# Performance work log

Hardware: AMD Instinct MI355X
Metric: run time of the kernel (lower is better)

The kernel has to match this reference:

```python
import jax, jax.numpy as jnp
from jax import lax
import numpy as np

KAPPA_S = 6.0
KAPPA_D = 5.0
POLICY_STRETCH = 2.0
VALUE_STRETCH = 1.0 / 32.0
VALUE_GAUGE = 0.2

RAW_PATTERNS = [
    [[0, 0, 0, 0, -5, 1, 1, 1, 1], [0, 0, 0, 0, -5, -5, -5, -5, -5], 0],
    [[0, 0, 0, 1, -5, 1, 1, 1, 0], [0, 0, 0, -5, -5, -5, -5, -5, 0], 0],
    [[0, 0, 1, 1, -5, 1, 1, 0, 0], [0, 0, -5, -5, -5, -5, -5, 0, 0], 0],
    [[0, 1, 1, 1, -5, 1, 0, 0, 0], [0, -5, -5, -5, -5, -5, 0, 0, 0], 0],
    [[1, 1, 1, 1, -5, 0, 0, 0, 0], [-5, -5, -5, -5, -5, 0, 0, 0, 0], 0],
    [[0, -5, 1, 1, 1, 1, 1, -5, 0], [0, 0, -5, -5, -5, -5, -5, 0, 0], -4],
]


def _all_3xnxn(p3):
    # Lay a 9-long 1D pattern (one per input channel) along the 4 line
    # directions (horizontal, vertical, two diagonals) of a 9x9 kernel.
    f = np.zeros((9, 9, 3, 4), np.float32)
    for ch in range(3):
        v = np.asarray(p3[ch], np.float32)
        f[4, :, ch, 0] = v                       # horizontal
        f[:, 4, ch, 1] = v                       # vertical
        for i in range(9):
            f[i, i, ch, 2] = v[i]                # main diagonal
            f[i, 8 - i, ch, 3] = v[i]            # anti diagonal
    return f


def _assemble_filters():
    # select_patterns: channel 0 -> [offense, defense, defense]; channel 1 -> [defense, offense, defense]
    patterns = []
    for off, de, bias in RAW_PATTERNS:
        patterns.append(([off, de, de], bias))
        patterns.append(([de, off, de], bias))
    filt = np.stack([_all_3xnxn(p) for p, _ in patterns], axis=3)  # (9,9,3,12,4)
    filt = np.reshape(filt, (9, 9, 3, -1))                          # filter idx = 4*pattern + direction
    biases = np.asarray([b for _, b in patterns for _ in range(4)], np.float32)
    return jnp.asarray(filt), jnp.asarray(biases)


def _safe_pow(x, p):
    # x >= 0 everywhere it is used; guards the grad of x**p (p<1) at x==0.
    pos = x > 0
    return jnp.where(pos, jnp.where(pos, x, 1.0) ** p, 0.0)


def setup_inputs() -> dict:
    key = jax.random.key(0)
    state = jax.random.normal(key, (4096, 19, 19, 3), dtype=jnp.float32)
    W, b = _assemble_filters()
    return {"state": state, "W": W, "b": b}


def reference(state, W, b):
    # detector: Conv2D 9x9, 48 filters, SAME padding, relu
    counts = jax.nn.relu(
        lax.conv_general_dilated(
            state, W, window_strides=(1, 1), padding="SAME",
            dimension_numbers=("NHWC", "HWIO", "NHWC"),
        ) + b
    )  # [B, N, N, 48]
    # peel: 3x3 conv with identity-center kernel, VALID padding == crop of 1
    core = counts[:, 1:-1, 1:-1, :]  # [B, N-2, N-2, 48]
    B, H, Wd, _ = core.shape
    # filter index = 8*shift + 4*channel + direction for the 40 line filters
    core40 = core[..., :40].reshape(B, H, Wd, 5, 2, 4)  # (shift, channel, direction)
    s = jnp.sum(core40 ** KAPPA_S, axis=3)               # sum over shifts -> [B,H,W,2,4]
    sd = jnp.sum(_safe_pow(s, KAPPA_D / KAPPA_S), axis=4)  # sum over directions -> [B,H,W,2]
    f = _safe_pow(sd, 1.0 / KAPPA_D)                     # [B,H,W,2]; [...,c] = field(channel c)
    f_cur, f_oth = f[..., 0], f[..., 1]
    logits = (f_cur + f_oth).reshape(B, -1)
    probs = jax.nn.softmax(POLICY_STRETCH * logits, axis=-1)
    raw_value = VALUE_GAUGE * (jnp.sum(f_cur, axis=(1, 2)) - jnp.sum(f_oth, axis=(1, 2)))
    value = jnp.tanh(VALUE_STRETCH * raw_value)
    return probs, value
```

## Files before the change

kernel.cpp:

```cpp
#include <hip/hip_runtime.h>
#include <math.h>


__device__ __forceinline__ float fpow(float x, float e) {
    float r = __builtin_amdgcn_exp2f(e * __builtin_amdgcn_logf(x));
    return (x > 0.f) ? r : 0.f;
}
__device__ __forceinline__ float fexp(float x) {
    return __builtin_amdgcn_exp2f(x * 1.44269504088896f);
}

#define SLAB 1024
#define C_OFF 729

__global__ __launch_bounds__(256) void topo_policy_value(
    const float* __restrict__ state,
    float* __restrict__ probs,
    float* __restrict__ value,
    int nb)
{
    __shared__ float2 l2[4 * SLAB];

    const int tid  = threadIdx.x;
    const int wv   = tid >> 6;
    const int lane = tid & 63;
    const int b    = blockIdx.x * 4 + wv;
    if (b >= nb) return;
    float2* s2 = l2 + wv * SLAB;

    const float* src = state + (size_t)b * (19 * 19 * 3);

    #pragma unroll
    for (int it = 0; it < 12; ++it) {
        int j = lane + it * 64;
        if (j < 729) {
            int py = j / 27, px = j - py * 27;
            int r = py - 4, c = px - 4;
            float l0 = 0.f, l1 = 0.f, lv = 0.f;
            if ((unsigned)r < 19u && (unsigned)c < 19u) {
                int o = 3 * (r * 19 + c);
                l0 = src[o]; l1 = src[o + 1]; lv = src[o + 2];
            }
            s2[j] = make_float2(fmaf(-5.f, l1 + lv, l0),
                                fmaf(-5.f, l0 + lv, l1));
        }
    }
    #pragma unroll
    for (int it = 0; it < 5; ++it) {
        int j = lane + it * 64;
        if (j < 289) {
            int y = j / 17, x = j - y * 17;
            int o = 3 * ((y + 1) * 19 + (x + 1));
            s2[C_OFF + j] = make_float2(6.f * src[o], 6.f * src[o + 1]);
        }
    }
    __builtin_amdgcn_s_waitcnt(0);
    __builtin_amdgcn_wave_barrier();

    float g[5], es[5];
    float dif = 0.f;
    #pragma unroll
    for (int k = 0; k < 5; ++k) {
        int p = lane + 64 * k;
        float gk = -3.0e38f;
        if (p < 289) {
            int y = p / 17, x = p - y * 17;
            float2 h = s2[C_OFF + p];
            int c0 = (y + 5) * 27 + (x + 1);
            int c1 = (y + 1) * 27 + (x + 5);
            int c2 = (y + 1) * 27 + (x + 1);
            int c3 = (y + 1) * 27 + (x + 9);
            float sd0 = 0.f, sd1 = 0.f;
            #define ORIENT(BASE, STEP)                                      \
            {                                                               \
                float2 e[9];                                                \
                _Pragma("unroll")                                           \
                for (int i = 0; i < 9; ++i) e[i] = s2[(BASE) + i * (STEP)]; \
                float wx = e[4].x + e[5].x + e[6].x + e[7].x + e[8].x;      \
                float wy = e[4].y + e[5].y + e[6].y + e[7].y + e[8].y;      \
                float t0 = 0.f, t1 = 0.f;                                   \
                _Pragma("unroll")                                           \
                for (int pp = 0; pp < 5; ++pp) {                            \
                    float a0 = fmaxf(wx - h.x, 0.f);                        \
                    float a1 = fmaxf(wy - h.y, 0.f);                        \
                    float q0 = a0 * a0, q1 = a1 * a1;                       \
                    t0 = fmaf(q0 * q0, q0, t0);                             \
                    t1 = fmaf(q1 * q1, q1, t1);                             \
                    if (pp < 4) {                                           \
                        wx += e[3 - pp].x - e[8 - pp].x;                    \
                        wy += e[3 - pp].y - e[8 - pp].y;                    \
                    }                                                       \
                }                                                           \
                sd0 += fpow(t0, 5.0f / 6.0f);                               \
                sd1 += fpow(t1, 5.0f / 6.0f);                               \
            }
            ORIENT(c0, 1)
            ORIENT(c1, 27)
            ORIENT(c2, 28)
            ORIENT(c3, 26)
            #undef ORIENT
            float fc = fpow(sd0, 0.2f);
            float fo = fpow(sd1, 0.2f);
            gk = 2.f * (fc + fo);
            dif += fc - fo;
        }
        g[k] = gk;
    }

    float M = fmaxf(fmaxf(fmaxf(g[0], g[1]), fmaxf(g[2], g[3])), g[4]);
    #pragma unroll
    for (int off = 32; off > 0; off >>= 1)
        M = fmaxf(M, __shfl_xor(M, off, 64));

    float S = 0.f;
    #pragma unroll
    for (int k = 0; k < 5; ++k) {
        es[k] = (g[k] > -1.0e38f) ? fexp(g[k] - M) : 0.f;
        S += es[k];
    }
    #pragma unroll
    for (int off = 32; off > 0; off >>= 1) S += __shfl_xor(S, off, 64);
    #pragma unroll
    for (int off = 32; off > 0; off >>= 1) dif += __shfl_xor(dif, off, 64);

    const float invS = __builtin_amdgcn_rcpf(S);
    float* pout = probs + (size_t)b * 289;
    #pragma unroll
    for (int k = 0; k < 5; ++k) {
        int p = lane + 64 * k;
        if (p < 289) pout[p] = es[k] * invS;
    }
    if (lane == 0) {
        float z = dif * (0.2f / 32.0f);
        float t = __builtin_amdgcn_exp2f(z * (2.0f * 1.44269504088896f));
        value[b] = (t - 1.f) * __builtin_amdgcn_rcpf(t + 1.f);
    }
}

extern "C" void kernel_launch(void* const* d_in, const int* in_sizes, int n_in,
                              void* d_out, int out_size, void* d_ws, size_t ws_size,
                              hipStream_t stream) {
    const float* state = (const float*)d_in[0];
    const int nb = in_sizes[0] / (19 * 19 * 3);
    float* probs = (float*)d_out;
    float* value = probs + (size_t)nb * 289;
    const int grid = (nb + 3) / 4;
    topo_policy_value<<<dim3(grid), dim3(256), 0, stream>>>(state, probs, value, nb);
}
```

Baseline: 84.29 us.

## Map one board per block with one thread per board position

```diff
diff --git a/kernel.cpp b/kernel.cpp
--- a/kernel.cpp
+++ b/kernel.cpp
@@ -13,26 +13,65 @@
 #define SLAB 1024
 #define C_OFF 729
 
-__global__ __launch_bounds__(256) void topo_policy_value(
+__device__ __forceinline__ float2 eval_pos(const float2* __restrict__ s2, int p)
+{
+    int y = p / 17, x = p - y * 17;
+    float2 h = s2[C_OFF + p];
+    int c0 = (y + 5) * 27 + (x + 1);
+    int c1 = (y + 1) * 27 + (x + 5);
+    int c2 = (y + 1) * 27 + (x + 1);
+    int c3 = (y + 1) * 27 + (x + 9);
+    float sd0 = 0.f, sd1 = 0.f;
+    #define ORIENT(BASE, STEP)                                      \
+    {                                                               \
+        float2 e[9];                                                \
+        _Pragma("unroll")                                           \
+        for (int i = 0; i < 9; ++i) e[i] = s2[(BASE) + i * (STEP)]; \
+        float wx = e[4].x + e[5].x + e[6].x + e[7].x + e[8].x;      \
+        float wy = e[4].y + e[5].y + e[6].y + e[7].y + e[8].y;      \
+        float t0 = 0.f, t1 = 0.f;                                   \
+        _Pragma("unroll")                                           \
+        for (int pp = 0; pp < 5; ++pp) {                            \
+            float a0 = fmaxf(wx - h.x, 0.f);                        \
+            float a1 = fmaxf(wy - h.y, 0.f);                        \
+            float q0 = a0 * a0, q1 = a1 * a1;                       \
+            t0 = fmaf(q0 * q0, q0, t0);                             \
+            t1 = fmaf(q1 * q1, q1, t1);                             \
+            if (pp < 4) {                                           \
+                wx += e[3 - pp].x - e[8 - pp].x;                    \
+                wy += e[3 - pp].y - e[8 - pp].y;                    \
+            }                                                       \
+        }                                                           \
+        sd0 += fpow(t0, 5.0f / 6.0f);                               \
+        sd1 += fpow(t1, 5.0f / 6.0f);                               \
+    }
+    ORIENT(c0, 1)
+    ORIENT(c1, 27)
+    ORIENT(c2, 28)
+    ORIENT(c3, 26)
+    #undef ORIENT
+    return make_float2(fpow(sd0, 0.2f), fpow(sd1, 0.2f));
+}
+
+__global__ __launch_bounds__(256, 6) void topo_policy_value(
     const float* __restrict__ state,
     float* __restrict__ probs,
     float* __restrict__ value,
     int nb)
 {
-    __shared__ float2 l2[4 * SLAB];
+    __shared__ float2 s2[SLAB];
+    __shared__ float red[4][3];
 
     const int tid  = threadIdx.x;
     const int wv   = tid >> 6;
     const int lane = tid & 63;
-    const int b    = blockIdx.x * 4 + wv;
-    if (b >= nb) return;
-    float2* s2 = l2 + wv * SLAB;
+    const int b    = blockIdx.x;
 
     const float* src = state + (size_t)b * (19 * 19 * 3);
 
     #pragma unroll
-    for (int it = 0; it < 12; ++it) {
-        int j = lane + it * 64;
+    for (int it = 0; it < 3; ++it) {
+        int j = tid + it * 256;
         if (j < 729) {
             int py = j / 27, px = j - py * 27;
             int r = py - 4, c = px - 4;
@@ -46,92 +85,57 @@
         }
     }
     #pragma unroll
-    for (int it = 0; it < 5; ++it) {
-        int j = lane + it * 64;
+    for (int it = 0; it < 2; ++it) {
+        int j = tid + it * 256;
         if (j < 289) {
             int y = j / 17, x = j - y * 17;
             int o = 3 * ((y + 1) * 19 + (x + 1));
             s2[C_OFF + j] = make_float2(6.f * src[o], 6.f * src[o + 1]);
         }
     }
-    __builtin_amdgcn_s_waitcnt(0);
-    __builtin_amdgcn_wave_barrier();
+    __syncthreads();
 
-    float g[5], es[5];
     float dif = 0.f;
-    #pragma unroll
-    for (int k = 0; k < 5; ++k) {
-        int p = lane + 64 * k;
-        float gk = -3.0e38f;
-        if (p < 289) {
-            int y = p / 17, x = p - y * 17;
-            float2 h = s2[C_OFF + p];
-            int c0 = (y + 5) * 27 + (x + 1);
-            int c1 = (y + 1) * 27 + (x + 5);
-            int c2 = (y + 1) * 27 + (x + 1);
-            int c3 = (y + 1) * 27 + (x + 9);
-            float sd0 = 0.f, sd1 = 0.f;
-            #define ORIENT(BASE, STEP)                                      \
-            {                                                               \
-                float2 e[9];                                                \
-                _Pragma("unroll")                                           \
-                for (int i = 0; i < 9; ++i) e[i] = s2[(BASE) + i * (STEP)]; \
-                float wx = e[4].x + e[5].x + e[6].x + e[7].x + e[8].x;      \
-                float wy = e[4].y + e[5].y + e[6].y + e[7].y + e[8].y;      \
-                float t0 = 0.f, t1 = 0.f;                                   \
-                _Pragma("unroll")                                           \
-                for (int pp = 0; pp < 5; ++pp) {                            \
-                    float a0 = fmaxf(wx - h.x, 0.f);                        \
-                    float a1 = fmaxf(wy - h.y, 0.f);                        \
-                    float q0 = a0 * a0, q1 = a1 * a1;                       \
-                    t0 = fmaf(q0 * q0, q0, t0);                             \
-                    t1 = fmaf(q1 * q1, q1, t1);                             \
-                    if (pp < 4) {                                           \
-                        wx += e[3 - pp].x - e[8 - pp].x;                    \
-                        wy += e[3 - pp].y - e[8 - pp].y;                    \
-                    }                                                       \
-                }                                                           \
-                sd0 += fpow(t0, 5.0f / 6.0f);                               \
-                sd1 += fpow(t1, 5.0f / 6.0f);                               \
-            }
-            ORIENT(c0, 1)
-            ORIENT(c1, 27)
-            ORIENT(c2, 28)
-            ORIENT(c3, 26)
-            #undef ORIENT
-            float fc = fpow(sd0, 0.2f);
-            float fo = fpow(sd1, 0.2f);
-            gk = 2.f * (fc + fo);
-            dif += fc - fo;
-        }
-        g[k] = gk;
+    float gA, gB = -3.0e38f;
+    {
+        float2 r = eval_pos(s2, tid);
+        gA = 2.f * (r.x + r.y);
+        dif += r.x - r.y;
+    }
+    const bool hasB = (wv == 3) && (lane < 33);
+    if (hasB) {
+        float2 r = eval_pos(s2, 256 + lane);
+        gB = 2.f * (r.x + r.y);
+        dif += r.x - r.y;
     }
 
-    float M = fmaxf(fmaxf(fmaxf(g[0], g[1]), fmaxf(g[2], g[3])), g[4]);
+    float Mw = fmaxf(gA, gB);
     #pragma unroll
     for (int off = 32; off > 0; off >>= 1)
-        M = fmaxf(M, __shfl_xor(M, off, 64));
+        Mw = fmaxf(Mw, __shfl_xor(Mw, off, 64));
+    if (lane == 0) red[wv][0] = Mw;
+    __syncthreads();
+    const float M = fmaxf(fmaxf(red[0][0], red[1][0]),
+                          fmaxf(red[2][0], red[3][0]));
 
-    float S = 0.f;
+    float esA = fexp(gA - M);
+    float esB = hasB ? fexp(gB - M) : 0.f;
+    float Sw = esA + esB;
     #pragma unroll
-    for (int k = 0; k < 5; ++k) {
-        es[k] = (g[k] > -1.0e38f) ? fexp(g[k] - M) : 0.f;
-        S += es[k];
-    }
-    #pragma unroll
-    for (int off = 32; off > 0; off >>= 1) S += __shfl_xor(S, off, 64);
+    for (int off = 32; off > 0; off >>= 1) Sw += __shfl_xor(Sw, off, 64);
     #pragma unroll
     for (int off = 32; off > 0; off >>= 1) dif += __shfl_xor(dif, off, 64);
+    if (lane == 0) { red[wv][1] = Sw; red[wv][2] = dif; }
+    __syncthreads();
+    const float S = (red[0][1] + red[1][1]) + (red[2][1] + red[3][1]);
 
     const float invS = __builtin_amdgcn_rcpf(S);
     float* pout = probs + (size_t)b * 289;
-    #pragma unroll
-    for (int k = 0; k < 5; ++k) {
-        int p = lane + 64 * k;
-        if (p < 289) pout[p] = es[k] * invS;
-    }
-    if (lane == 0) {
-        float z = dif * (0.2f / 32.0f);
+    pout[tid] = esA * invS;
+    if (hasB) pout[256 + lane] = esB * invS;
+    if (tid == 0) {
+        float df = (red[0][2] + red[1][2]) + (red[2][2] + red[3][2]);
+        float z = df * (0.2f / 32.0f);
         float t = __builtin_amdgcn_exp2f(z * (2.0f * 1.44269504088896f));
         value[b] = (t - 1.f) * __builtin_amdgcn_rcpf(t + 1.f);
     }
@@ -144,6 +148,5 @@
     const int nb = in_sizes[0] / (19 * 19 * 3);
     float* probs = (float*)d_out;
     float* value = probs + (size_t)nb * 289;
-    const int grid = (nb + 3) / 4;
-    topo_policy_value<<<dim3(grid), dim3(256), 0, stream>>>(state, probs, value, nb);
+    topo_policy_value<<<dim3(nb), dim3(256), 0, stream>>>(state, probs, value, nb);
 }
```

Measured after the change: 85.39 us. No clear change (+1.3%).
